# Kernel optimization log

Measured on AMD Instinct MI355X. Metric: run time of the kernel, lower is better.

## Reference

```python
import jax, jax.numpy as jnp
import numpy as np

B, N, E, H, HEADS = 4, 10000, 160000, 128, 4
NEG_SLOPE = 0.2  # PyG GATConv default
LN_EPS = 1e-5


def setup_inputs() -> dict:
    key = jax.random.key(0)
    ks = jax.random.split(key, 24)
    inp = {}
    inp["node_embeddings"] = jax.random.normal(ks[0], (B, N, H), dtype=jnp.float32)
    inp["src_index"] = jax.random.randint(ks[1], (B, E), 0, N)
    inp["tgt_index"] = jax.random.randint(ks[2], (B, E), 0, N)
    sc = 1.0 / np.sqrt(H)
    for i in range(3):
        j = 3 + 3 * i
        inp[f"W{i+1}"] = jax.random.normal(ks[j], (H, HEADS * H), dtype=jnp.float32) * sc
        inp[f"att_src{i+1}"] = jax.random.normal(ks[j + 1], (HEADS, H), dtype=jnp.float32) * sc
        inp[f"att_dst{i+1}"] = jax.random.normal(ks[j + 2], (HEADS, H), dtype=jnp.float32) * sc
        inp[f"bias{i+1}"] = jnp.zeros((H,), dtype=jnp.float32)
    inp["ln1_g"] = jnp.ones((H,), dtype=jnp.float32)
    inp["ln1_b"] = jnp.zeros((H,), dtype=jnp.float32)
    inp["ln2_g"] = jnp.ones((H,), dtype=jnp.float32)
    inp["ln2_b"] = jnp.zeros((H,), dtype=jnp.float32)
    return inp


def _layer_norm(x, g, b):
    mu = jnp.mean(x, axis=-1, keepdims=True)
    var = jnp.mean((x - mu) ** 2, axis=-1, keepdims=True)
    return (x - mu) * jax.lax.rsqrt(var + LN_EPS) * g + b


def _gat(x, src, tgt, W, a_s, a_d, b):
    # x: [N, H]; src/tgt: [E'] (self-loops already appended). eval mode -> no dropout.
    h = (x @ W).reshape(N, HEADS, H)               # [N, heads, H]
    e_src = jnp.einsum('nhc,hc->nh', h, a_s)       # [N, heads]
    e_dst = jnp.einsum('nhc,hc->nh', h, a_d)
    e = jax.nn.leaky_relu(e_src[src] + e_dst[tgt], NEG_SLOPE)  # [E', heads]
    m = jax.ops.segment_max(e, tgt, num_segments=N)            # per-target max
    ex = jnp.exp(e - m[tgt])
    s = jax.ops.segment_sum(ex, tgt, num_segments=N)
    alpha = ex / s[tgt]                                        # [E', heads]
    out = jax.ops.segment_sum(alpha[:, :, None] * h[src], tgt, num_segments=N)
    return out.mean(axis=1) + b                                # concat=False -> head mean


def reference(node_embeddings, src_index, tgt_index,
              W1, att_src1, att_dst1, bias1,
              W2, att_src2, att_dst2, bias2,
              W3, att_src3, att_dst3, bias3,
              ln1_g, ln1_b, ln2_g, ln2_b):
    loop = jnp.arange(N, dtype=src_index.dtype)

    def one_graph(x, src, tgt):
        s = jnp.concatenate([src, loop])   # GATConv add_self_loops=True (default)
        t = jnp.concatenate([tgt, loop])
        m = _gat(x, s, t, W1, att_src1, att_dst1, bias1)
        m = jax.nn.relu(_layer_norm(m, ln1_g, ln1_b))
        m = _gat(m, s, t, W2, att_src2, att_dst2, bias2)
        m = jax.nn.relu(_layer_norm(m, ln2_g, ln2_b))
        m = _gat(m, s, t, W3, att_src3, att_dst3, bias3)
        return m

    return jax.vmap(one_graph)(node_embeddings, src_index, tgt_index)
```

## Files before the change

### kernel.cpp

```cpp
#include <hip/hip_runtime.h>
#include <hip/hip_bf16.h>
#include <cstdint>
#include <cstddef>

#define B_ 4
#define N_ 10000
#define E_ 160000
#define H_ 128
#define HEADS_ 4
#define HH_ 512
#define NROWS (B_*N_)

typedef __attribute__((ext_vector_type(8))) short bf16x8;
typedef __attribute__((ext_vector_type(4))) float f32x4;
typedef __attribute__((ext_vector_type(2))) float f32x2;

__device__ __forceinline__ float lrelu(float x){ return x > 0.f ? x : 0.2f*x; }
__device__ __forceinline__ unsigned short f2b(float f){
  unsigned int u = __builtin_bit_cast(unsigned int, f);
  unsigned int r = (u + 0x7fffu + ((u >> 16) & 1u)) >> 16;
  return (unsigned short)r;
}
__device__ __forceinline__ float blo(unsigned int u){ return __builtin_bit_cast(float, u << 16); }
__device__ __forceinline__ float bhi(unsigned int u){ return __builtin_bit_cast(float, u & 0xffff0000u); }

__device__ __forceinline__ void acc_row(f32x2* ac, float al, uint4 h){
  f32x2 v = {al, al};
  ac[0] += v * (f32x2){blo(h.x), bhi(h.x)};
  ac[1] += v * (f32x2){blo(h.y), bhi(h.y)};
  ac[2] += v * (f32x2){blo(h.z), bhi(h.z)};
  ac[3] += v * (f32x2){blo(h.w), bhi(h.w)};
}

__global__ void k_count(const int* __restrict__ tgt, int* __restrict__ cnt){
  int e = blockIdx.x*blockDim.x + threadIdx.x;
  int b = blockIdx.y;
  int t = tgt[(size_t)b*E_ + e];
  atomicAdd(&cnt[b*N_ + t], 1);
}

__global__ void k_scan(const int* __restrict__ cnt, int* __restrict__ off, int* __restrict__ cursor){
  int b = blockIdx.x;
  __shared__ int wsum[16];
  __shared__ int carry_s;
  int lane = threadIdx.x & 63, wid = threadIdx.x >> 6;
  if (threadIdx.x == 0){ carry_s = 0; off[b*(N_+1)] = 0; }
  __syncthreads();
  for (int base = 0; base < N_; base += 1024){
    int i = base + threadIdx.x;
    int v = (i < N_) ? cnt[b*N_ + i] : 0;
    int x = v;
    #pragma unroll
    for (int d = 1; d < 64; d <<= 1){
      int y = __shfl_up(x, d);
      if (lane >= d) x += y;
    }
    if (lane == 63) wsum[wid] = x;
    __syncthreads();
    if (wid == 0 && lane < 16){
      int w = wsum[lane];
      #pragma unroll
      for (int d = 1; d < 16; d <<= 1){
        int y = __shfl_up(w, d, 16);
        if (lane >= d) w += y;
      }
      wsum[lane] = w;
    }
    __syncthreads();
    int excl = (wid ? wsum[wid-1] : 0) + carry_s;
    if (i < N_){
      int inc = x + excl;
      off[b*(N_+1) + i + 1] = inc;
      cursor[b*N_ + i] = inc - v;
    }
    __syncthreads();
    if (threadIdx.x == 0) carry_s += wsum[15];
    __syncthreads();
  }
}

__global__ void k_scatter(const int* __restrict__ src, const int* __restrict__ tgt,
                          int* __restrict__ cursor, int* __restrict__ csr){
  int e = blockIdx.x*blockDim.x + threadIdx.x;
  int b = blockIdx.y;
  int t = tgt[(size_t)b*E_ + e];
  int pos = atomicAdd(&cursor[b*N_ + t], 1);
  csr[(size_t)b*E_ + pos] = src[(size_t)b*E_ + e];
}

__global__ void k_prep(const float* __restrict__ W0, const float* __restrict__ W1, const float* __restrict__ W2,
                       const float* __restrict__ as0, const float* __restrict__ as1, const float* __restrict__ as2,
                       const float* __restrict__ ad0, const float* __restrict__ ad1, const float* __restrict__ ad2,
                       float* __restrict__ wasA, float* __restrict__ wadA, unsigned short* __restrict__ wtA){
  int l = blockIdx.y;
  const float* W   = (l==0)?W0:(l==1)?W1:W2;
  const float* asp = (l==0)?as0:(l==1)?as1:as2;
  const float* adp = (l==0)?ad0:(l==1)?ad1:ad2;
  if (blockIdx.x < 256){
    int i = blockIdx.x*256 + threadIdx.x;
    int c = i >> 7, k = i & 127;
    wtA[(size_t)l*HH_*H_ + i] = f2b(W[(size_t)k*HH_ + c]);
  } else {
    int j = (blockIdx.x - 256)*256 + threadIdx.x;
    if (j < H_*HEADS_){
      int k = j >> 2, h = j & 3;
      const float* wrow = W + (size_t)k*HH_ + h*H_;
      const float* asr = asp + h*H_;
      const float* adr = adp + h*H_;
      float ss = 0.f, sd = 0.f;
      for (int c = 0; c < H_; ++c){ float w = wrow[c]; ss += w*asr[c]; sd += w*adr[c]; }
      wasA[l*HH_ + j] = ss; wadA[l*HH_ + j] = sd;
    }
  }
}

__global__ __launch_bounds__(256) void k_cast_logits(const float* __restrict__ X,
    const float* __restrict__ was, const float* __restrict__ wad,
    unsigned short* __restrict__ Xb, float* __restrict__ es, float* __restrict__ ed){
  int gw = (blockIdx.x*blockDim.x + threadIdx.x) >> 6;
  int lane = threadIdx.x & 63;
  float2 v = *(const float2*)(X + (size_t)gw*H_ + lane*2);
  unsigned int o = ((unsigned int)f2b(v.y) << 16) | (unsigned int)f2b(v.x);
  *(unsigned int*)(Xb + (size_t)gw*H_ + lane*2) = o;
  int c = lane*2;
  const f32x4* w4 = (const f32x4*)was;
  const f32x4* d4 = (const f32x4*)wad;
  f32x4 se = v.x*w4[c] + v.y*w4[c+1];
  f32x4 de = v.x*d4[c] + v.y*d4[c+1];
  #pragma unroll
  for (int d = 1; d < 64; d <<= 1){
    se.x += __shfl_xor(se.x,d); se.y += __shfl_xor(se.y,d);
    se.z += __shfl_xor(se.z,d); se.w += __shfl_xor(se.w,d);
    de.x += __shfl_xor(de.x,d); de.y += __shfl_xor(de.y,d);
    de.z += __shfl_xor(de.z,d); de.w += __shfl_xor(de.w,d);
  }
  if (lane == 0){
    *(float4*)(es + (size_t)gw*4) = make_float4(se.x, se.y, se.z, se.w);
    *(float4*)(ed + (size_t)gw*4) = make_float4(de.x, de.y, de.z, de.w);
  }
}

__global__ __launch_bounds__(256) void k_gemm_mfma(const unsigned short* __restrict__ Xb,
    const unsigned short* __restrict__ Wt, unsigned short* __restrict__ Hb){
  __shared__ unsigned short xs[64*128];
  __shared__ unsigned short ws[64*128];
  int row0 = blockIdx.x * 64, col0 = blockIdx.y * 64;
  int tid = threadIdx.x;
  int ch = tid & 15, r0 = tid >> 4;
  #pragma unroll
  for (int p = 0; p < 4; ++p){
    int r = r0 + p*16;
    int sc = ch ^ (r & 7);
    *(uint4*)(&xs[r*128 + sc*8]) = *(const uint4*)(Xb + (size_t)(row0 + r)*H_ + ch*8);
    *(uint4*)(&ws[r*128 + sc*8]) = *(const uint4*)(Wt + (size_t)(col0 + r)*H_ + ch*8);
  }
  __syncthreads();
  int w = tid >> 6, l = tid & 63;
  int lr = l & 15, q = l >> 4;
  f32x4 z = {0.f, 0.f, 0.f, 0.f};
  f32x4 acc[4] = {z, z, z, z};
  int arow = w*16 + lr;
  #pragma unroll
  for (int kf = 0; kf < 4; ++kf){
    int bch = kf*4 + q;
    bf16x8 a = *(const bf16x8*)(&xs[arow*128 + (bch ^ (arow & 7))*8]);
    #pragma unroll
    for (int cf = 0; cf < 4; ++cf){
      int brow = cf*16 + lr;
      bf16x8 bfr = *(const bf16x8*)(&ws[brow*128 + (bch ^ (brow & 7))*8]);
      acc[cf] = __builtin_amdgcn_mfma_f32_16x16x32_bf16(a, bfr, acc[cf], 0, 0, 0);
    }
  }
  #pragma unroll
  for (int cf = 0; cf < 4; ++cf){
    #pragma unroll
    for (int rg = 0; rg < 4; ++rg){
      int row = row0 + w*16 + q*4 + rg;
      int col = col0 + cf*16 + lr;
      Hb[(size_t)row*HH_ + col] = f2b(acc[cf][rg]);
    }
  }
}

template<bool FINAL>
__global__ __launch_bounds__(256) void k_aggregate(
    const unsigned short* __restrict__ Hb,
    const float* __restrict__ es, const float* __restrict__ ed,
    const int* __restrict__ off, const int* __restrict__ csr,
    const float* __restrict__ bias,
    const float* __restrict__ wasN, const float* __restrict__ wadN,
    const float* __restrict__ lng, const float* __restrict__ lnb,
    float* __restrict__ Yout, unsigned short* __restrict__ Xbout,
    float* __restrict__ esN, float* __restrict__ edN)
{
  __shared__ float part_s[2][16][8];
  __shared__ float orow_s[2][128];
  int wv = threadIdx.x >> 6, lane = threadIdx.x & 63;
  int nd = wv >> 1;
  int pw = wv & 1;
  int gw = blockIdx.x*2 + nd;
  int b = gw / N_, t = gw - b*N_;
  const float4 edv = *(const float4*)(ed + (size_t)gw*4);
  int start = off[b*(N_+1) + t];
  int deg = off[b*(N_+1) + t + 1] - start;
  int total = deg + 1;
  const int* lst = csr + (size_t)b*E_ + start;
  const float* esb = es + (size_t)b*N_*4;
  int head = lane >> 4;
  int cb = head*H_ + (lane & 15)*8;
  const unsigned short* hbase = Hb + (size_t)b*N_*HH_;
  float edh = head==0 ? edv.x : head==1 ? edv.y : head==2 ? edv.z : edv.w;
  float Mh, rSh;

  if (total <= 64){
    bool valid = lane < total;
    int srcn = (lane < deg) ? lst[lane] : t;
    float4 ev = *(const float4*)(esb + (size_t)srcn*4);
    float e0 = valid ? lrelu(ev.x + edv.x) : -1e30f;
    float e1 = valid ? lrelu(ev.y + edv.y) : -1e30f;
    float e2 = valid ? lrelu(ev.z + edv.z) : -1e30f;
    float e3 = valid ? lrelu(ev.w + edv.w) : -1e30f;
    float M0 = e0, M1 = e1, M2 = e2, M3 = e3;
    #pragma unroll
    for (int d = 1; d < 64; d <<= 1){
      M0 = fmaxf(M0, __shfl_xor(M0, d)); M1 = fmaxf(M1, __shfl_xor(M1, d));
      M2 = fmaxf(M2, __shfl_xor(M2, d)); M3 = fmaxf(M3, __shfl_xor(M3, d));
    }
    float p0 = valid ? __expf(e0 - M0) : 0.f;
    float p1 = valid ? __expf(e1 - M1) : 0.f;
    float p2 = valid ? __expf(e2 - M2) : 0.f;
    float p3 = valid ? __expf(e3 - M3) : 0.f;
    float S0 = p0, S1 = p1, S2 = p2, S3 = p3;
    #pragma unroll
    for (int d = 1; d < 64; d <<= 1){
      S0 += __shfl_xor(S0, d); S1 += __shfl_xor(S1, d);
      S2 += __shfl_xor(S2, d); S3 += __shfl_xor(S3, d);
    }
    Mh = head==0 ? M0 : head==1 ? M1 : head==2 ? M2 : M3;
    float Sh = head==0 ? S0 : head==1 ? S1 : head==2 ? S2 : S3;
    rSh = 1.0f / Sh;
  } else {
    float m0=-1e30f, m1=-1e30f, m2=-1e30f, m3=-1e30f;
    float s0=0.f, s1=0.f, s2=0.f, s3=0.f;
    for (int i2 = lane; i2 <= deg; i2 += 64){
      int srcn = (i2 < deg) ? lst[i2] : t;
      float4 ev = *(const float4*)(esb + (size_t)srcn*4);
      float e0 = lrelu(ev.x + edv.x);
      float e1 = lrelu(ev.y + edv.y);
      float e2 = lrelu(ev.z + edv.z);
      float e3 = lrelu(ev.w + edv.w);
      float nm;
      nm = fmaxf(m0, e0); s0 = s0*__expf(m0-nm) + __expf(e0-nm); m0 = nm;
      nm = fmaxf(m1, e1); s1 = s1*__expf(m1-nm) + __expf(e1-nm); m1 = nm;
      nm = fmaxf(m2, e2); s2 = s2*__expf(m2-nm) + __expf(e2-nm); m2 = nm;
      nm = fmaxf(m3, e3); s3 = s3*__expf(m3-nm) + __expf(e3-nm); m3 = nm;
    }
    #pragma unroll
    for (int d = 1; d < 64; d <<= 1){
      float om, os, nm;
      om = __shfl_xor(m0, d); os = __shfl_xor(s0, d); nm = fmaxf(m0, om);
      s0 = s0*__expf(m0-nm) + os*__expf(om-nm); m0 = nm;
      om = __shfl_xor(m1, d); os = __shfl_xor(s1, d); nm = fmaxf(m1, om);
      s1 = s1*__expf(m1-nm) + os*__expf(om-nm); m1 = nm;
      om = __shfl_xor(m2, d); os = __shfl_xor(s2, d); nm = fmaxf(m2, om);
      s2 = s2*__expf(m2-nm) + os*__expf(om-nm); m2 = nm;
      om = __shfl_xor(m3, d); os = __shfl_xor(s3, d); nm = fmaxf(m3, om);
      s3 = s3*__expf(m3-nm) + os*__expf(om-nm); m3 = nm;
    }
    Mh = head==0 ? m0 : head==1 ? m1 : head==2 ? m2 : m3;
    float Sh = head==0 ? s0 : head==1 ? s1 : head==2 ? s2 : s3;
    rSh = 1.0f / Sh;
  }

  f32x2 zz = {0.f, 0.f};
  f32x2 ac[4] = {zz, zz, zz, zz};
  int i = pw;
  for (; i + 2 < total; i += 4){
    int sA = lst[i];
    int sB = (i + 2 < deg) ? lst[i+2] : t;
    float eA = esb[(size_t)sA*4 + head];
    float eB = esb[(size_t)sB*4 + head];
    uint4 hA = *(const uint4*)(hbase + (size_t)sA*HH_ + cb);
    uint4 hB = *(const uint4*)(hbase + (size_t)sB*HH_ + cb);
    float aA = __expf(lrelu(eA + edh) - Mh) * rSh;
    float aB = __expf(lrelu(eB + edh) - Mh) * rSh;
    acc_row(ac, aA, hA);
    acc_row(ac, aB, hB);
  }
  if (i < total){
    int sA = (i < deg) ? lst[i] : t;
    float eA = esb[(size_t)sA*4 + head];
    uint4 hA = *(const uint4*)(hbase + (size_t)sA*HH_ + cb);
    float aA = __expf(lrelu(eA + edh) - Mh) * rSh;
    acc_row(ac, aA, hA);
  }

  float a[8] = {ac[0].x, ac[0].y, ac[1].x, ac[1].y, ac[2].x, ac[2].y, ac[3].x, ac[3].y};
  #pragma unroll
  for (int d = 16; d < 64; d <<= 1)
    #pragma unroll
    for (int j = 0; j < 8; j++) a[j] += __shfl_xor(a[j], d);

  if (pw == 1 && lane < 16){
    #pragma unroll
    for (int j = 0; j < 8; j++) part_s[nd][lane][j] = a[j];
  }
  __syncthreads();

  int c = (lane & 15)*8;
  if (pw == 0){
    float tot[8];
    if (lane < 16){
      #pragma unroll
      for (int j = 0; j < 8; j++) tot[j] = a[j] + part_s[nd][lane][j];
    }
    if (FINAL){
      if (lane < 16){
        float4 o0 = make_float4(0.25f*tot[0]+bias[c+0], 0.25f*tot[1]+bias[c+1],
                                0.25f*tot[2]+bias[c+2], 0.25f*tot[3]+bias[c+3]);
        float4 o1 = make_float4(0.25f*tot[4]+bias[c+4], 0.25f*tot[5]+bias[c+5],
                                0.25f*tot[6]+bias[c+6], 0.25f*tot[7]+bias[c+7]);
        *(float4*)(Yout + (size_t)gw*H_ + c)     = o0;
        *(float4*)(Yout + (size_t)gw*H_ + c + 4) = o1;
      }
    } else {
      float o[8];
      float ss = 0.f;
      if (lane < 16){
        #pragma unroll
        for (int j = 0; j < 8; j++){ o[j] = 0.25f*tot[j] + bias[c+j]; ss += o[j]; }
      }
      #pragma unroll
      for (int d = 1; d < 16; d <<= 1) ss += __shfl_xor(ss, d);
      float mu = ss * (1.f/H_);
      float vv = 0.f;
      if (lane < 16){
        #pragma unroll
        for (int j = 0; j < 8; j++){ float dx = o[j]-mu; vv += dx*dx; }
      }
      #pragma unroll
      for (int d = 1; d < 16; d <<= 1) vv += __shfl_xor(vv, d);
      float inv = rsqrtf(vv*(1.f/H_) + 1e-5f);
      if (lane < 16){
        float4 g0 = *(const float4*)(lng + c), g1 = *(const float4*)(lng + c + 4);
        float4 b0 = *(const float4*)(lnb + c), b1 = *(const float4*)(lnb + c + 4);
        float gg[8] = {g0.x,g0.y,g0.z,g0.w,g1.x,g1.y,g1.z,g1.w};
        float bb[8] = {b0.x,b0.y,b0.z,b0.w,b1.x,b1.y,b1.z,b1.w};
        float oo[8];
        #pragma unroll
        for (int j = 0; j < 8; j++) oo[j] = fmaxf((o[j]-mu)*inv*gg[j] + bb[j], 0.f);
        uint4 up;
        up.x = ((unsigned int)f2b(oo[1]) << 16) | f2b(oo[0]);
        up.y = ((unsigned int)f2b(oo[3]) << 16) | f2b(oo[2]);
        up.z = ((unsigned int)f2b(oo[5]) << 16) | f2b(oo[4]);
        up.w = ((unsigned int)f2b(oo[7]) << 16) | f2b(oo[6]);
        *(uint4*)(Xbout + (size_t)gw*H_ + lane*8) = up;
        *(float4*)(&orow_s[nd][c])     = make_float4(oo[0], oo[1], oo[2], oo[3]);
        *(float4*)(&orow_s[nd][c + 4]) = make_float4(oo[4], oo[5], oo[6], oo[7]);
      }
      __builtin_amdgcn_wave_barrier();
      float pe = 0.f, pd = 0.f;
      #pragma unroll
      for (int j = 0; j < 8; j++){
        float xv = orow_s[nd][c + j];
        pe += xv * wasN[(c + j)*4 + head];
        pd += xv * wadN[(c + j)*4 + head];
      }
      #pragma unroll
      for (int d = 1; d < 16; d <<= 1){ pe += __shfl_xor(pe, d); pd += __shfl_xor(pd, d); }
      if ((lane & 15) == 0){
        esN[(size_t)gw*4 + head] = pe;
        edN[(size_t)gw*4 + head] = pd;
      }
    }
  }
}

extern "C" void kernel_launch(void* const* d_in, const int* in_sizes, int n_in,
                              void* d_out, int out_size, void* d_ws, size_t ws_size,
                              hipStream_t stream){
  const float* x0   = (const float*)d_in[0];
  const int*   srcI = (const int*)d_in[1];
  const int*   tgtI = (const int*)d_in[2];
  const float* Wl[3]  = {(const float*)d_in[3], (const float*)d_in[7],  (const float*)d_in[11]};
  const float* asl[3] = {(const float*)d_in[4], (const float*)d_in[8],  (const float*)d_in[12]};
  const float* adl[3] = {(const float*)d_in[5], (const float*)d_in[9],  (const float*)d_in[13]};
  const float* bl[3]  = {(const float*)d_in[6], (const float*)d_in[10], (const float*)d_in[14]};
  const float* lng[2] = {(const float*)d_in[15], (const float*)d_in[17]};
  const float* lnb[2] = {(const float*)d_in[16], (const float*)d_in[18]};

  char* p = (char*)d_ws;
  auto carve = [&](size_t bytes) -> void* {
    void* r = (void*)p; p += (bytes + 255) & ~(size_t)255; return r;
  };
  int*   off    = (int*)carve((size_t)B_*(N_+1)*4);
  int*   cnt    = (int*)carve((size_t)B_*N_*4);
  int*   cursor = (int*)carve((size_t)B_*N_*4);
  int*   csr    = (int*)carve((size_t)B_*E_*4);
  float* es2[2] = {(float*)carve((size_t)NROWS*4*4), (float*)carve((size_t)NROWS*4*4)};
  float* ed2[2] = {(float*)carve((size_t)NROWS*4*4), (float*)carve((size_t)NROWS*4*4)};
  float* wasA   = (float*)carve((size_t)3*HH_*4);
  float* wadA   = (float*)carve((size_t)3*HH_*4);
  unsigned short* wtA  = (unsigned short*)carve((size_t)3*HH_*H_*2);
  unsigned short* hbuf = (unsigned short*)carve((size_t)NROWS*HH_*2);
  unsigned short* xbf  = (unsigned short*)carve((size_t)NROWS*H_*2);

  hipMemsetAsync(cnt, 0, (size_t)B_*N_*4, stream);
  k_count  <<<dim3(E_/256, B_), 256, 0, stream>>>(tgtI, cnt);
  k_scan   <<<B_, 1024, 0, stream>>>(cnt, off, cursor);
  k_scatter<<<dim3(E_/256, B_), 256, 0, stream>>>(srcI, tgtI, cursor, csr);
  k_prep   <<<dim3(258, 3), 256, 0, stream>>>(Wl[0], Wl[1], Wl[2],
                                              asl[0], asl[1], asl[2],
                                              adl[0], adl[1], adl[2],
                                              wasA, wadA, wtA);
  k_cast_logits<<<NROWS/4, 256, 0, stream>>>(x0, wasA, wadA, xbf, es2[0], ed2[0]);

  for (int l = 0; l < 3; ++l){
    k_gemm_mfma<<<dim3(NROWS/64, HH_/64), 256, 0, stream>>>(xbf, wtA + (size_t)l*HH_*H_, hbuf);
    int cur = l & 1, nxt = cur ^ 1;
    if (l < 2){
      k_aggregate<false><<<NROWS/2, 256, 0, stream>>>(hbuf, es2[cur], ed2[cur], off, csr, bl[l],
          wasA + (size_t)(l+1)*HH_, wadA + (size_t)(l+1)*HH_, lng[l], lnb[l],
          nullptr, xbf, es2[nxt], ed2[nxt]);
    } else {
      k_aggregate<true><<<NROWS/2, 256, 0, stream>>>(hbuf, es2[cur], ed2[cur], off, csr, bl[l],
          nullptr, nullptr, nullptr, nullptr,
          (float*)d_out, nullptr, nullptr, nullptr);
    }
  }
}
```

Measured before the change: 543.0 us.

## Assign one wave per target node in aggregate, dropping cross-wave reduction

```diff
diff --git a/kernel.cpp b/kernel.cpp
--- a/kernel.cpp
+++ b/kernel.cpp
@@ -15,7 +15,7 @@
 typedef __attribute__((ext_vector_type(4))) float f32x4;
 typedef __attribute__((ext_vector_type(2))) float f32x2;
 
-__device__ __forceinline__ float lrelu(float x){ return x > 0.f ? x : 0.2f*x; }
+__device__ __forceinline__ float lrelu(float x){ return fmaxf(x, 0.2f*x); }
 __device__ __forceinline__ unsigned short f2b(float f){
   unsigned int u = __builtin_bit_cast(unsigned int, f);
   unsigned int r = (u + 0x7fffu + ((u >> 16) & 1u)) >> 16;
@@ -193,12 +193,9 @@
     float* __restrict__ Yout, unsigned short* __restrict__ Xbout,
     float* __restrict__ esN, float* __restrict__ edN)
 {
-  __shared__ float part_s[2][16][8];
-  __shared__ float orow_s[2][128];
+  __shared__ float orow_s[4][128];
   int wv = threadIdx.x >> 6, lane = threadIdx.x & 63;
-  int nd = wv >> 1;
-  int pw = wv & 1;
-  int gw = blockIdx.x*2 + nd;
+  int gw = blockIdx.x*4 + wv;
   int b = gw / N_, t = gw - b*N_;
   const float4 edv = *(const float4*)(ed + (size_t)gw*4);
   int start = off[b*(N_+1) + t];
@@ -210,7 +207,7 @@
   int cb = head*H_ + (lane & 15)*8;
   const unsigned short* hbase = Hb + (size_t)b*N_*HH_;
   float edh = head==0 ? edv.x : head==1 ? edv.y : head==2 ? edv.z : edv.w;
-  float Mh, rSh;
+  float Lh;
 
   if (total <= 64){
     bool valid = lane < total;
@@ -236,9 +233,9 @@
       S0 += __shfl_xor(S0, d); S1 += __shfl_xor(S1, d);
       S2 += __shfl_xor(S2, d); S3 += __shfl_xor(S3, d);
     }
-    Mh = head==0 ? M0 : head==1 ? M1 : head==2 ? M2 : M3;
+    float Mh = head==0 ? M0 : head==1 ? M1 : head==2 ? M2 : M3;
     float Sh = head==0 ? S0 : head==1 ? S1 : head==2 ? S2 : S3;
-    rSh = 1.0f / Sh;
+    Lh = Mh + __logf(Sh);
   } else {
     float m0=-1e30f, m1=-1e30f, m2=-1e30f, m3=-1e30f;
     float s0=0.f, s1=0.f, s2=0.f, s3=0.f;
@@ -267,23 +264,23 @@
       om = __shfl_xor(m3, d); os = __shfl_xor(s3, d); nm = fmaxf(m3, om);
       s3 = s3*__expf(m3-nm) + os*__expf(om-nm); m3 = nm;
     }
-    Mh = head==0 ? m0 : head==1 ? m1 : head==2 ? m2 : m3;
+    float Mh = head==0 ? m0 : head==1 ? m1 : head==2 ? m2 : m3;
     float Sh = head==0 ? s0 : head==1 ? s1 : head==2 ? s2 : s3;
-    rSh = 1.0f / Sh;
+    Lh = Mh + __logf(Sh);
   }
 
   f32x2 zz = {0.f, 0.f};
   f32x2 ac[4] = {zz, zz, zz, zz};
-  int i = pw;
-  for (; i + 2 < total; i += 4){
+  int i = 0;
+  for (; i + 1 < total; i += 2){
     int sA = lst[i];
-    int sB = (i + 2 < deg) ? lst[i+2] : t;
+    int sB = (i + 1 < deg) ? lst[i+1] : t;
     float eA = esb[(size_t)sA*4 + head];
     float eB = esb[(size_t)sB*4 + head];
     uint4 hA = *(const uint4*)(hbase + (size_t)sA*HH_ + cb);
     uint4 hB = *(const uint4*)(hbase + (size_t)sB*HH_ + cb);
-    float aA = __expf(lrelu(eA + edh) - Mh) * rSh;
-    float aB = __expf(lrelu(eB + edh) - Mh) * rSh;
+    float aA = __expf(lrelu(eA + edh) - Lh);
+    float aB = __expf(lrelu(eB + edh) - Lh);
     acc_row(ac, aA, hA);
     acc_row(ac, aB, hB);
   }
@@ -291,7 +288,7 @@
     int sA = (i < deg) ? lst[i] : t;
     float eA = esb[(size_t)sA*4 + head];
     uint4 hA = *(const uint4*)(hbase + (size_t)sA*HH_ + cb);
-    float aA = __expf(lrelu(eA + edh) - Mh) * rSh;
+    float aA = __expf(lrelu(eA + edh) - Lh);
     acc_row(ac, aA, hA);
   }
 
@@ -301,77 +298,62 @@
     #pragma unroll
     for (int j = 0; j < 8; j++) a[j] += __shfl_xor(a[j], d);
 
-  if (pw == 1 && lane < 16){
-    #pragma unroll
-    for (int j = 0; j < 8; j++) part_s[nd][lane][j] = a[j];
-  }
-  __syncthreads();
-
   int c = (lane & 15)*8;
-  if (pw == 0){
-    float tot[8];
+  if (FINAL){
     if (lane < 16){
-      #pragma unroll
-      for (int j = 0; j < 8; j++) tot[j] = a[j] + part_s[nd][lane][j];
-    }
-    if (FINAL){
-      if (lane < 16){
-        float4 o0 = make_float4(0.25f*tot[0]+bias[c+0], 0.25f*tot[1]+bias[c+1],
-                                0.25f*tot[2]+bias[c+2], 0.25f*tot[3]+bias[c+3]);
-        float4 o1 = make_float4(0.25f*tot[4]+bias[c+4], 0.25f*tot[5]+bias[c+5],
-                                0.25f*tot[6]+bias[c+6], 0.25f*tot[7]+bias[c+7]);
-        *(float4*)(Yout + (size_t)gw*H_ + c)     = o0;
-        *(float4*)(Yout + (size_t)gw*H_ + c + 4) = o1;
-      }
-    } else {
-      float o[8];
-      float ss = 0.f;
-      if (lane < 16){
-        #pragma unroll
-        for (int j = 0; j < 8; j++){ o[j] = 0.25f*tot[j] + bias[c+j]; ss += o[j]; }
-      }
-      #pragma unroll
-      for (int d = 1; d < 16; d <<= 1) ss += __shfl_xor(ss, d);
-      float mu = ss * (1.f/H_);
-      float vv = 0.f;
-      if (lane < 16){
-        #pragma unroll
-        for (int j = 0; j < 8; j++){ float dx = o[j]-mu; vv += dx*dx; }
-      }
-      #pragma unroll
-      for (int d = 1; d < 16; d <<= 1) vv += __shfl_xor(vv, d);
-      float inv = rsqrtf(vv*(1.f/H_) + 1e-5f);
-      if (lane < 16){
-        float4 g0 = *(const float4*)(lng + c), g1 = *(const float4*)(lng + c + 4);
-        float4 b0 = *(const float4*)(lnb + c), b1 = *(const float4*)(lnb + c + 4);
-        float gg[8] = {g0.x,g0.y,g0.z,g0.w,g1.x,g1.y,g1.z,g1.w};
-        float bb[8] = {b0.x,b0.y,b0.z,b0.w,b1.x,b1.y,b1.z,b1.w};
-        float oo[8];
-        #pragma unroll
-        for (int j = 0; j < 8; j++) oo[j] = fmaxf((o[j]-mu)*inv*gg[j] + bb[j], 0.f);
-        uint4 up;
-        up.x = ((unsigned int)f2b(oo[1]) << 16) | f2b(oo[0]);
-        up.y = ((unsigned int)f2b(oo[3]) << 16) | f2b(oo[2]);
-        up.z = ((unsigned int)f2b(oo[5]) << 16) | f2b(oo[4]);
-        up.w = ((unsigned int)f2b(oo[7]) << 16) | f2b(oo[6]);
-        *(uint4*)(Xbout + (size_t)gw*H_ + lane*8) = up;
-        *(float4*)(&orow_s[nd][c])     = make_float4(oo[0], oo[1], oo[2], oo[3]);
-        *(float4*)(&orow_s[nd][c + 4]) = make_float4(oo[4], oo[5], oo[6], oo[7]);
-      }
-      __builtin_amdgcn_wave_barrier();
-      float pe = 0.f, pd = 0.f;
-      #pragma unroll
-      for (int j = 0; j < 8; j++){
-        float xv = orow_s[nd][c + j];
-        pe += xv * wasN[(c + j)*4 + head];
-        pd += xv * wadN[(c + j)*4 + head];
-      }
-      #pragma unroll
-      for (int d = 1; d < 16; d <<= 1){ pe += __shfl_xor(pe, d); pd += __shfl_xor(pd, d); }
-      if ((lane & 15) == 0){
-        esN[(size_t)gw*4 + head] = pe;
-        edN[(size_t)gw*4 + head] = pd;
-      }
+      float4 o0 = make_float4(0.25f*a[0]+bias[c+0], 0.25f*a[1]+bias[c+1],
+                              0.25f*a[2]+bias[c+2], 0.25f*a[3]+bias[c+3]);
+      float4 o1 = make_float4(0.25f*a[4]+bias[c+4], 0.25f*a[5]+bias[c+5],
+                              0.25f*a[6]+bias[c+6], 0.25f*a[7]+bias[c+7]);
+      *(float4*)(Yout + (size_t)gw*H_ + c)     = o0;
+      *(float4*)(Yout + (size_t)gw*H_ + c + 4) = o1;
+    }
+  } else {
+    float o[8];
+    #pragma unroll
+    for (int j = 0; j < 8; j++) o[j] = 0.25f*a[j] + bias[c+j];
+    float ss = 0.f;
+    #pragma unroll
+    for (int j = 0; j < 8; j++) ss += o[j];
+    #pragma unroll
+    for (int d = 1; d < 16; d <<= 1) ss += __shfl_xor(ss, d);
+    float mu = ss * (1.f/H_);
+    float vv = 0.f;
+    #pragma unroll
+    for (int j = 0; j < 8; j++){ float dx = o[j]-mu; vv += dx*dx; }
+    #pragma unroll
+    for (int d = 1; d < 16; d <<= 1) vv += __shfl_xor(vv, d);
+    float inv = rsqrtf(vv*(1.f/H_) + 1e-5f);
+    float4 g0 = *(const float4*)(lng + c), g1 = *(const float4*)(lng + c + 4);
+    float4 b0 = *(const float4*)(lnb + c), b1 = *(const float4*)(lnb + c + 4);
+    float gg[8] = {g0.x,g0.y,g0.z,g0.w,g1.x,g1.y,g1.z,g1.w};
+    float bb[8] = {b0.x,b0.y,b0.z,b0.w,b1.x,b1.y,b1.z,b1.w};
+    float oo[8];
+    #pragma unroll
+    for (int j = 0; j < 8; j++) oo[j] = fmaxf((o[j]-mu)*inv*gg[j] + bb[j], 0.f);
+    if (lane < 16){
+      uint4 up;
+      up.x = ((unsigned int)f2b(oo[1]) << 16) | f2b(oo[0]);
+      up.y = ((unsigned int)f2b(oo[3]) << 16) | f2b(oo[2]);
+      up.z = ((unsigned int)f2b(oo[5]) << 16) | f2b(oo[4]);
+      up.w = ((unsigned int)f2b(oo[7]) << 16) | f2b(oo[6]);
+      *(uint4*)(Xbout + (size_t)gw*H_ + lane*8) = up;
+      *(float4*)(&orow_s[wv][c])     = make_float4(oo[0], oo[1], oo[2], oo[3]);
+      *(float4*)(&orow_s[wv][c + 4]) = make_float4(oo[4], oo[5], oo[6], oo[7]);
+    }
+    __builtin_amdgcn_wave_barrier();
+    float pe = 0.f, pd = 0.f;
+    #pragma unroll
+    for (int j = 0; j < 8; j++){
+      float xv = orow_s[wv][c + j];
+      pe += xv * wasN[(c + j)*4 + head];
+      pd += xv * wadN[(c + j)*4 + head];
+    }
+    #pragma unroll
+    for (int d = 1; d < 16; d <<= 1){ pe += __shfl_xor(pe, d); pd += __shfl_xor(pd, d); }
+    if ((lane & 15) == 0){
+      esN[(size_t)gw*4 + head] = pe;
+      edN[(size_t)gw*4 + head] = pd;
     }
   }
 }
@@ -419,11 +401,11 @@
     k_gemm_mfma<<<dim3(NROWS/64, HH_/64), 256, 0, stream>>>(xbf, wtA + (size_t)l*HH_*H_, hbuf);
     int cur = l & 1, nxt = cur ^ 1;
     if (l < 2){
-      k_aggregate<false><<<NROWS/2, 256, 0, stream>>>(hbuf, es2[cur], ed2[cur], off, csr, bl[l],
+      k_aggregate<false><<<NROWS/4, 256, 0, stream>>>(hbuf, es2[cur], ed2[cur], off, csr, bl[l],
           wasA + (size_t)(l+1)*HH_, wadA + (size_t)(l+1)*HH_, lng[l], lnb[l],
           nullptr, xbf, es2[nxt], ed2[nxt]);
     } else {
-      k_aggregate<true><<<NROWS/2, 256, 0, stream>>>(hbuf, es2[cur], ed2[cur], off, csr, bl[l],
+      k_aggregate<true><<<NROWS/4, 256, 0, stream>>>(hbuf, es2[cur], ed2[cur], off, csr, bl[l],
           nullptr, nullptr, nullptr, nullptr,
           (float*)d_out, nullptr, nullptr, nullptr);
     }
```

Result: faster. 511.0 us (-5.9%).
